# Performance work log

Hardware: AMD Instinct MI355X
Metric: run time of the kernel (lower is better)

Reference implementation:

```python
import jax, jax.numpy as jnp
import numpy as np

D = 1024
H = 16
HD = D // H
DFF = 4 * D
LN_EPS = 1e-5

def layernorm(x, gamma, beta):
    mu = jnp.mean(x, axis=-1, keepdims=True)
    var = jnp.mean(jnp.square(x - mu), axis=-1, keepdims=True)
    return (x - mu) * jax.lax.rsqrt(var + LN_EPS) * gamma + beta

def setup_inputs() -> dict:
    key = jax.random.key(0)
    ks = jax.random.split(key, 10)
    B, Nq, Nk = 2, 2048, 2048
    s = 0.02
    return {
        "q_x": jax.random.normal(ks[0], (B, Nq, D), jnp.float32),
        "kv_x": jax.random.normal(ks[1], (B, Nk, D), jnp.float32),
        "Wq": jax.random.normal(ks[2], (D, D), jnp.float32) * s,
        "Wkv": jax.random.normal(ks[3], (2 * D, D), jnp.float32) * s,
        "Wo": jax.random.normal(ks[4], (D, D), jnp.float32) * s,
        "bo": jnp.zeros((D,), jnp.float32),
        "ln_q_g": jnp.ones((D,), jnp.float32),
        "ln_q_b": jnp.zeros((D,), jnp.float32),
        "ln_kv_g": jnp.ones((D,), jnp.float32),
        "ln_kv_b": jnp.zeros((D,), jnp.float32),
        "W1": jax.random.normal(ks[5], (DFF, D), jnp.float32) * s,
        "b1": jnp.zeros((DFF,), jnp.float32),
        "W2": jax.random.normal(ks[6], (D, DFF), jnp.float32) * s,
        "b2": jnp.zeros((D,), jnp.float32),
    }

def reference(q_x, kv_x, Wq, Wkv, Wo, bo, ln_q_g, ln_q_b, ln_kv_g, ln_kv_b, W1, b1, W2, b2):
    B, Nq, _ = q_x.shape
    Nk = kv_x.shape[1]
    scale = HD ** -0.5
    # norm + projections
    q = layernorm(q_x, ln_q_g, ln_q_b) @ Wq.T                    # [B,Nq,D]
    kv = layernorm(kv_x, ln_kv_g, ln_kv_b) @ Wkv.T               # [B,Nk,2D]
    q = q.reshape(B, Nq, H, HD).transpose(0, 2, 1, 3)            # [B,H,Nq,hd]
    kv = kv.reshape(B, Nk, 2, H, HD).transpose(2, 0, 3, 1, 4)    # [2,B,H,Nk,hd]
    k, v = kv[0], kv[1]
    attn = jnp.einsum('bhqd,bhkd->bhqk', q, k) * scale           # [B,H,Nq,Nk]
    attn = jax.nn.softmax(attn, axis=-1)
    out = jnp.einsum('bhqk,bhkd->bhqd', attn, v)
    out = out.transpose(0, 2, 1, 3).reshape(B, Nq, D)
    x = q_x + out @ Wo.T + bo
    h = jax.nn.silu(x @ W1.T + b1)
    x = x + h @ W2.T + b2
    return x
```

## Files before the change

kernel.cpp:

```cpp
#include <hip/hip_runtime.h>

using u16   = unsigned short;
using f32x4 = __attribute__((ext_vector_type(4))) float;
using s16x8 = __attribute__((ext_vector_type(8))) short;
using u32x2 = __attribute__((ext_vector_type(2))) unsigned int;
using u32x4 = __attribute__((ext_vector_type(4))) unsigned int;

#define LOG2E 1.44269504088896f

static __device__ __forceinline__ u16 f2bf(float f) {
  union { float f; unsigned u; } a; a.f = f;
  unsigned r = a.u + 0x7fffu + ((a.u >> 16) & 1u);
  return (u16)(r >> 16);
}
static __device__ __forceinline__ unsigned cvtpk(float lo, float hi) {
  unsigned r;
  asm("v_cvt_pk_bf16_f32 %0, %1, %2" : "=v"(r) : "v"(lo), "v"(hi));
  return r;
}

static __device__ __forceinline__ void gload16(const void* g, void* l) {
  __builtin_amdgcn_global_load_lds(
      (__attribute__((address_space(1))) unsigned int*)g,
      (__attribute__((address_space(3))) unsigned int*)l, 16, 0, 0);
}

static __device__ __forceinline__ int xcd_swz(int b, int nb) {
  return (b & 7) * (nb >> 3) + (b >> 3);
}

__global__ __launch_bounds__(256) void prep_k(
    const float* __restrict__ Wq, const float* __restrict__ Wkv,
    const float* __restrict__ Wo, const float* __restrict__ W1,
    const float* __restrict__ W2,
    u16* __restrict__ wq_b, u16* __restrict__ wkv_b, u16* __restrict__ wo_b,
    u16* __restrict__ w1_b, u16* __restrict__ w2_b,
    const float* __restrict__ xq, const float* __restrict__ xk,
    const float* __restrict__ gq, const float* __restrict__ bq,
    const float* __restrict__ gk, const float* __restrict__ bk,
    u16* __restrict__ oq, u16* __restrict__ ok)
{
  const int blk = blockIdx.x, t = threadIdx.x;
  if (blk < 12288) {
    const int i = blk * 256 + t;
    const float* src; u16* dst; int off; float sc = 1.0f;
    if      (i <  262144) { src = Wq;  dst = wq_b;  off = i; sc = 0.125f * LOG2E; }
    else if (i <  786432) { src = Wkv; dst = wkv_b; off = i -  262144; }
    else if (i < 1048576) { src = Wo;  dst = wo_b;  off = i -  786432; }
    else if (i < 2097152) { src = W1;  dst = w1_b;  off = i - 1048576; }
    else                  { src = W2;  dst = w2_b;  off = i - 2097152; }
    const float4 v = ((const float4*)src)[off];
    ushort4 o;
    o.x = f2bf(v.x * sc); o.y = f2bf(v.y * sc); o.z = f2bf(v.z * sc); o.w = f2bf(v.w * sc);
    ((ushort4*)dst)[off] = o;
    return;
  }
  int row = blk - 12288;
  const float* x; const float* gam; const float* bet; u16* out;
  if (row < 4096) { x = xq; gam = gq; bet = bq; out = oq; }
  else { row -= 4096; x = xk; gam = gk; bet = bk; out = ok; }
  const float4 v = ((const float4*)(x + (size_t)row * 1024))[t];
  float s  = v.x + v.y + v.z + v.w;
  float ss = v.x*v.x + v.y*v.y + v.z*v.z + v.w*v.w;
  #pragma unroll
  for (int m = 1; m < 64; m <<= 1) { s += __shfl_xor(s, m); ss += __shfl_xor(ss, m); }
  __shared__ float red[8];
  const int w = t >> 6;
  if ((t & 63) == 0) { red[w] = s; red[4 + w] = ss; }
  __syncthreads();
  s  = red[0] + red[1] + red[2] + red[3];
  ss = red[4] + red[5] + red[6] + red[7];
  const float mu   = s * (1.0f / 1024.0f);
  const float rstd = rsqrtf(ss * (1.0f / 1024.0f) - mu * mu + 1e-5f);
  const float4 gv = ((const float4*)gam)[t];
  const float4 bv = ((const float4*)bet)[t];
  ushort4 o;
  o.x = f2bf((v.x - mu) * rstd * gv.x + bv.x);
  o.y = f2bf((v.y - mu) * rstd * gv.y + bv.y);
  o.z = f2bf((v.z - mu) * rstd * gv.z + bv.z);
  o.w = f2bf((v.w - mu) * rstd * gv.w + bv.w);
  ((ushort4*)(out + (size_t)row * 1024))[t] = o;
}

template<int BIAS, int RES, int SILU, int OF32, int OBF>
static __device__ __forceinline__ void gemm_body64_2buf(
    const u16* __restrict__ A, const u16* __restrict__ B,
    u16* __restrict__ Cb, float* __restrict__ Cf,
    const float* __restrict__ bias, const float* __restrict__ resid,
    int N, int K, int bid, u16* smem)
{
  const int tid = threadIdx.x;
  const int w = tid >> 6, l = tid & 63;
  const int g = l >> 4, q = l & 15;
  const int ntn = N >> 6;
  const int bm = bid / ntn, bn = bid - bm * ntn;
  const int wr = w >> 1, wc = w & 1;
  const int sw = (q & 7) << 4;
  f32x4 acc[2][2] = {};

  const size_t abase = (size_t)(bm * 128) * K;
  const size_t bbase = (size_t)(bn * 64) * K;

  auto stage = [&](int buf, int k0) {
    u16* as = smem + buf * 8192;
    u16* bs = smem + 16384 + buf * 4096;
    #pragma unroll
    for (int r = 0; r < 2; ++r) {
      const int c = (r << 9) + tid;
      const int row = c >> 3;
      const int sp = (c & 7) ^ (row & 7);
      gload16(A + abase + (size_t)row * K + k0 + sp * 8,
              as + (size_t)((r << 9) + (w << 6)) * 8);
    }
    const int row = tid >> 3;
    const int sp = (tid & 7) ^ (row & 7);
    gload16(B + bbase + (size_t)row * K + k0 + sp * 8,
            bs + (size_t)(w << 6) * 8);
  };

  const int NT = K >> 6;
  stage(0, 0);
  asm volatile("s_waitcnt vmcnt(0)" ::: "memory");
  __syncthreads();
  int cur = 0;
  for (int t = 0; t < NT; ++t) {
    if (t + 1 < NT) stage(cur ^ 1, (t + 1) << 6);
    const char* as = (const char*)(smem + cur * 8192);
    const char* bs = (const char*)(smem + 16384 + cur * 4096);
    #pragma unroll
    for (int ks = 0; ks < 2; ++ks) {
      s16x8 af[2], bfr[2];
      #pragma unroll
      for (int m = 0; m < 2; ++m)
        af[m] = *(const s16x8*)(as + (size_t)(wr * 32 + m * 16 + q) * 128 +
                                ((ks * 64 + g * 16) ^ sw));
      #pragma unroll
      for (int n = 0; n < 2; ++n)
        bfr[n] = *(const s16x8*)(bs + (size_t)(wc * 32 + n * 16 + q) * 128 +
                                 ((ks * 64 + g * 16) ^ sw));
      #pragma unroll
      for (int m = 0; m < 2; ++m)
        #pragma unroll
        for (int n = 0; n < 2; ++n)
          acc[m][n] = __builtin_amdgcn_mfma_f32_16x16x32_bf16(af[m], bfr[n], acc[m][n], 0, 0, 0);
    }
    asm volatile("s_waitcnt vmcnt(0)" ::: "memory");
    __syncthreads();
    cur ^= 1;
  }

  #pragma unroll
  for (int m = 0; m < 2; ++m) {
    const int row0 = bm * 128 + wr * 32 + m * 16 + g * 4;
    #pragma unroll
    for (int n = 0; n < 2; ++n) {
      const int col = bn * 64 + wc * 32 + n * 16 + q;
      float bv = 0.0f;
      if (BIAS) bv = bias[col];
      #pragma unroll
      for (int r = 0; r < 4; ++r) {
        const size_t idx = (size_t)(row0 + r) * N + col;
        float v = acc[m][n][r] + bv;
        if (RES)  v += resid[idx];
        if (SILU) v = v / (1.0f + __expf(-v));
        if (OF32) Cf[idx] = v;
        if (OBF)  Cb[idx] = f2bf(v);
      }
    }
  }
}

template<int BIAS, int RES, int SILU, int OF32, int OBF>
__global__ __launch_bounds__(512, 4) void gemm_k2(
    const u16* __restrict__ A, const u16* __restrict__ B,
    u16* __restrict__ Cb, float* __restrict__ Cf,
    const float* __restrict__ bias, const float* __restrict__ resid,
    int N, int K)
{
  __shared__ u16 smem[24576];
  const int bid = xcd_swz(blockIdx.x, gridDim.x);
  gemm_body64_2buf<BIAS, RES, SILU, OF32, OBF>(A, B, Cb, Cf, bias, resid, N, K, bid, smem);
}

__global__ __launch_bounds__(512, 4) void gemm_qkv_k(
    const u16* __restrict__ lnq, const u16* __restrict__ wq, u16* __restrict__ qp,
    const u16* __restrict__ lnk, const u16* __restrict__ wkv, u16* __restrict__ kvp)
{
  __shared__ u16 smem[24576];
  const int sbid = xcd_swz(blockIdx.x, 1536);
  if (sbid < 512)
    gemm_body64_2buf<0,0,0,0,1>(lnq, wq, qp, nullptr, nullptr, nullptr, 1024, 1024,
                                sbid, smem);
  else
    gemm_body64_2buf<0,0,0,0,1>(lnk, wkv, kvp, nullptr, nullptr, nullptr, 2048, 1024,
                                sbid - 512, smem);
}

template<int BIAS, int RES, int SILU, int OF32, int OBF>
__global__ __launch_bounds__(512, 4) void gemm_k3(
    const u16* __restrict__ A, const u16* __restrict__ B,
    u16* __restrict__ Cb, float* __restrict__ Cf,
    const float* __restrict__ bias, const float* __restrict__ resid,
    int N, int K)
{
  __shared__ u16 smem[36864];
  const int bid = xcd_swz(blockIdx.x, gridDim.x);
  const int tid = threadIdx.x;
  const int w = tid >> 6, l = tid & 63;
  const int g = l >> 4, q = l & 15;
  const int ntn = N >> 6;
  const int bm = bid / ntn, bn = bid - bm * ntn;
  const int wr = w >> 1, wc = w & 1;
  const int sw = (q & 7) << 4;
  f32x4 acc[2][2] = {};

  const size_t abase = (size_t)(bm * 128) * K;
  const size_t bbase = (size_t)(bn * 64) * K;

  const u16* pa0; const u16* pa1; const u16* pb;
  {
    const int r0 = tid >> 3, s0 = (tid & 7) ^ (r0 & 7);
    pa0 = A + abase + (size_t)r0 * K + s0 * 8;
    const int c1 = 512 + tid;
    const int r1 = c1 >> 3, s1 = (c1 & 7) ^ (r1 & 7);
    pa1 = A + abase + (size_t)r1 * K + s1 * 8;
    const int rb = tid >> 3, sb = (tid & 7) ^ (rb & 7);
    pb = B + bbase + (size_t)rb * K + sb * 8;
  }
  const int wdo = w * 512;

  auto stage = [&](int buf, int k0) {
    gload16(pa0 + k0, smem + buf * 8192 + wdo);
    gload16(pa1 + k0, smem + buf * 8192 + 4096 + wdo);
    gload16(pb  + k0, smem + 24576 + buf * 4096 + wdo);
  };

  const int NT = K >> 6;
  stage(0, 0);
  stage(1, 64);
  int cur = 0;
  for (int t = 0; t < NT; ++t) {
    if (t + 1 < NT) asm volatile("s_waitcnt vmcnt(3)" ::: "memory");
    else            asm volatile("s_waitcnt vmcnt(0)" ::: "memory");
    __builtin_amdgcn_s_barrier();
    asm volatile("" ::: "memory");
    if (t + 2 < NT) stage((cur == 0) ? 2 : cur - 1, (t + 2) << 6);

    const char* as = (const char*)(smem + cur * 8192);
    const char* bs = (const char*)(smem + 24576 + cur * 4096);
    #pragma unroll
    for (int ks = 0; ks < 2; ++ks) {
      s16x8 af[2], bfr[2];
      #pragma unroll
      for (int m = 0; m < 2; ++m)
        af[m] = *(const s16x8*)(as + (size_t)(wr * 32 + m * 16 + q) * 128 +
                                ((ks * 64 + g * 16) ^ sw));
      #pragma unroll
      for (int n = 0; n < 2; ++n)
        bfr[n] = *(const s16x8*)(bs + (size_t)(wc * 32 + n * 16 + q) * 128 +
                                 ((ks * 64 + g * 16) ^ sw));
      __builtin_amdgcn_s_setprio(1);
      #pragma unroll
      for (int m = 0; m < 2; ++m)
        #pragma unroll
        for (int n = 0; n < 2; ++n)
          acc[m][n] = __builtin_amdgcn_mfma_f32_16x16x32_bf16(af[m], bfr[n], acc[m][n], 0, 0, 0);
      __builtin_amdgcn_s_setprio(0);
    }
    cur = (cur == 2) ? 0 : cur + 1;
  }

  #pragma unroll
  for (int m = 0; m < 2; ++m) {
    const int row0 = bm * 128 + wr * 32 + m * 16 + g * 4;
    #pragma unroll
    for (int n = 0; n < 2; ++n) {
      const int col = bn * 64 + wc * 32 + n * 16 + q;
      float bv = 0.0f;
      if (BIAS) bv = bias[col];
      #pragma unroll
      for (int r = 0; r < 4; ++r) {
        const size_t idx = (size_t)(row0 + r) * N + col;
        float v = acc[m][n][r] + bv;
        if (RES)  v += resid[idx];
        if (SILU) v = v / (1.0f + __expf(-v));
        if (OF32) Cf[idx] = v;
        if (OBF)  Cb[idx] = f2bf(v);
      }
    }
  }
}

template<int BIAS, int RES, int SILU, int OF32, int OBF>
__global__ __launch_bounds__(512, 2) void gemm256_k(
    const u16* __restrict__ A, const u16* __restrict__ B,
    u16* __restrict__ Cb, float* __restrict__ Cf,
    const float* __restrict__ bias, const float* __restrict__ resid,
    int N, int K)
{
  __shared__ u16 smem[65536];
  char* smem_c = (char*)smem;
  const int tid = threadIdx.x;
  const int w = tid >> 6, l = tid & 63;
  const int g = l >> 4, q = l & 15;
  const int wm = w >> 2, wn = w & 3;
  const int ntn = N >> 8;
  const int bid = xcd_swz(blockIdx.x, gridDim.x);
  const int bm = bid / ntn, bn = bid - bm * ntn;

  const size_t abase = (size_t)(bm * 256) * K;
  const size_t bbase = (size_t)(bn * 256) * K;

  f32x4 acc[8][4] = {};

  auto stage2 = [&](int buf, int kt, int part) {
    const int isB = part & 1, khalf = part >> 1;
    #pragma unroll
    for (int sub = 0; sub < 2; ++sub) {
      const int row  = sub * 128 + (tid >> 2);
      const int slot = (tid & 3) ^ ((row >> 1) & 3);
      const u16* src = (isB ? B + bbase : A + abase)
                     + (size_t)row * K + kt * 64 + khalf * 32 + slot * 8;
      char* dst = smem_c + buf * 65536 + isB * 32768 + khalf * 16384
                + sub * 8192 + w * 1024;
      gload16(src, dst);
    }
  };

  const int NT = K >> 6;
  stage2(0, 0, 0); stage2(0, 0, 1); stage2(0, 0, 2); stage2(0, 0, 3);
  int cur = 0;
  const int so = (g ^ ((q >> 1) & 3)) * 16;
  for (int t = 0; t < NT; ++t) {
    const bool pre = (t + 1 < NT);
    const char* base = smem_c + cur * 65536;
    #pragma unroll
    for (int ks = 0; ks < 2; ++ks) {
      if (ks == 0 || pre) asm volatile("s_waitcnt vmcnt(4)" ::: "memory");
      else                asm volatile("s_waitcnt vmcnt(0)" ::: "memory");
      asm volatile("" ::: "memory");
      __builtin_amdgcn_s_barrier();
      asm volatile("" ::: "memory");
      const char* Ab = base + ks * 16384;
      const char* Bb = base + 32768 + ks * 16384;
      s16x8 af[8], bf0[2];
      #pragma unroll
      for (int m = 0; m < 8; ++m)
        af[m] = *(const s16x8*)(Ab + (wm * 128 + m * 16 + q) * 64 + so);
      #pragma unroll
      for (int n = 0; n < 2; ++n)
        bf0[n] = *(const s16x8*)(Bb + (wn * 64 + n * 16 + q) * 64 + so);
      if (pre) stage2(cur ^ 1, t + 1, ks * 2);
      asm volatile("s_waitcnt lgkmcnt(0)" ::: "memory");
      __builtin_amdgcn_sched_barrier(0);
      __builtin_amdgcn_s_setprio(1);
      #pragma unroll
      for (int m = 0; m < 8; ++m) {
        acc[m][0] = __builtin_amdgcn_mfma_f32_16x16x32_bf16(af[m], bf0[0], acc[m][0], 0, 0, 0);
        acc[m][1] = __builtin_amdgcn_mfma_f32_16x16x32_bf16(af[m], bf0[1], acc[m][1], 0, 0, 0);
      }
      __builtin_amdgcn_s_setprio(0);
      s16x8 bf1[2];
      #pragma unroll
      for (int n = 0; n < 2; ++n)
        bf1[n] = *(const s16x8*)(Bb + (wn * 64 + (2 + n) * 16 + q) * 64 + so);
      if (pre) stage2(cur ^ 1, t + 1, ks * 2 + 1);
      asm volatile("s_waitcnt lgkmcnt(0)" ::: "memory");
      __builtin_amdgcn_sched_barrier(0);
      __builtin_amdgcn_s_setprio(1);
      #pragma unroll
      for (int m = 0; m < 8; ++m) {
        acc[m][2] = __builtin_amdgcn_mfma_f32_16x16x32_bf16(af[m], bf1[0], acc[m][2], 0, 0, 0);
        acc[m][3] = __builtin_amdgcn_mfma_f32_16x16x32_bf16(af[m], bf1[1], acc[m][3], 0, 0, 0);
      }
      __builtin_amdgcn_s_setprio(0);
    }
    cur ^= 1;
  }

  #pragma unroll
  for (int m = 0; m < 8; ++m) {
    const int row0 = bm * 256 + wm * 128 + m * 16 + g * 4;
    #pragma unroll
    for (int n = 0; n < 4; ++n) {
      const int col = bn * 256 + wn * 64 + n * 16 + q;
      float bv = 0.0f;
      if (BIAS) bv = bias[col];
      #pragma unroll
      for (int r = 0; r < 4; ++r) {
        const size_t idx = (size_t)(row0 + r) * N + col;
        float v = acc[m][n][r] + bv;
        if (RES)  v += resid[idx];
        if (SILU) v = v / (1.0f + __expf(-v));
        if (OF32) Cf[idx] = v;
        if (OBF)  Cb[idx] = f2bf(v);
      }
    }
  }
}

__global__ __launch_bounds__(512, 4) void attn_k(
    const u16* __restrict__ Q, const u16* __restrict__ KV, u16* __restrict__ O)
{
  __shared__ u16 Ks[3][64 * 64];
  __shared__ u16 Vs[3][64 * 64];
  const int tid = threadIdx.x;
  const int w = tid >> 6, l = tid & 63;
  const int g = l >> 4, q = l & 15;
  const int idx = blockIdx.x >> 3;
  const int bh = (blockIdx.x & 7) * 4 + (idx >> 4);
  const int qt = idx & 15;
  const int b = bh >> 4, h = bh & 15;

  const size_t qrow = (size_t)(b * 2048 + qt * 128 + w * 16 + q);
  s16x8 qf[2];
  qf[0] = *(const s16x8*)&Q[qrow * 1024 + h * 64 + g * 8];
  qf[1] = *(const s16x8*)&Q[qrow * 1024 + h * 64 + 32 + g * 8];

  f32x4 oacc[4] = {};
  f32x4 ls = {0.0f, 0.0f, 0.0f, 0.0f};

  const u16* kvb = KV + (size_t)b * 2048 * 2048;
  const unsigned vs_base =
      (unsigned)(unsigned long long)(__attribute__((address_space(3))) u16*)Vs;

  const u16* pk; const u16* pv;
  {
    const int krow = tid >> 3, slot = tid & 7;
    pk = kvb + (size_t)krow * 2048 + h * 64 + ((slot ^ (krow & 7)) << 3);
    const int vkv = ((tid >> 3) & 15) * 4 + ((tid >> 1) & 3);
    const int vd0 = ((tid >> 7) & 3) * 16 + (tid & 1) * 8;
    pv = kvb + (size_t)vkv * 2048 + 1024 + h * 64 + vd0;
  }
  const int wdo = w * 512;

  auto stage = [&](int buf, int kv0) {
    const size_t off = (size_t)kv0 << 11;
    gload16(pk + off, &Ks[buf][0] + wdo);
    gload16(pv + off, &Vs[buf][0] + wdo);
  };

  stage(0, 0);
  stage(1, 64);
  int cur = 0;

  for (int kt = 0; kt < 32; ++kt) {
    if (kt < 31) asm volatile("s_waitcnt vmcnt(2)" ::: "memory");
    else         asm volatile("s_waitcnt vmcnt(0)" ::: "memory");
    __builtin_amdgcn_s_barrier();
    asm volatile("" ::: "memory");
    if (kt + 2 < 32) stage((cur == 0) ? 2 : cur - 1, (kt + 2) * 64);

    const char* ksb = (const char*)Ks[cur];
    f32x4 sacc[4] = {};
    __builtin_amdgcn_s_setprio(1);
    #pragma unroll
    for (int s = 0; s < 2; ++s)
      #pragma unroll
      for (int nf = 0; nf < 4; ++nf) {
        const int krw = nf * 16 + q;
        const s16x8 kf = *(const s16x8*)(ksb + krw * 128 +
                              ((s * 64 + g * 16) ^ ((krw & 7) << 4)));
        sacc[nf] = __builtin_amdgcn_mfma_f32_16x16x32_bf16(kf, qf[s], sacc[nf], 0, 0, 0);
      }
    __builtin_amdgcn_s_setprio(0);

    #pragma unroll
    for (int nf = 0; nf < 4; ++nf)
      #pragma unroll
      for (int r = 0; r < 4; ++r)
        sacc[nf][r] = __builtin_amdgcn_exp2f(sacc[nf][r]);
    ls += sacc[0]; ls += sacc[1]; ls += sacc[2]; ls += sacc[3];

    union { u32x4 u; s16x8 s8; } au[2];
    #pragma unroll
    for (int s = 0; s < 2; ++s) {
      au[s].u[0] = cvtpk(sacc[2*s  ][0], sacc[2*s  ][1]);
      au[s].u[1] = cvtpk(sacc[2*s  ][2], sacc[2*s  ][3]);
      au[s].u[2] = cvtpk(sacc[2*s+1][0], sacc[2*s+1][1]);
      au[s].u[3] = cvtpk(sacc[2*s+1][2], sacc[2*s+1][3]);
    }

    const unsigned a0 = vs_base + (unsigned)(cur * 8192) + (unsigned)(g * 128 + 2 * q);
    u32x2 v0,v1,v2,v3,v4,v5,v6,v7,v8,v9,v10,v11,v12,v13,v14,v15;
    asm volatile(
        "ds_read_b64_tr_b16 %0,  %16\n\t"
        "ds_read_b64_tr_b16 %1,  %16 offset:512\n\t"
        "ds_read_b64_tr_b16 %2,  %16 offset:2048\n\t"
        "ds_read_b64_tr_b16 %3,  %16 offset:2560\n\t"
        "ds_read_b64_tr_b16 %4,  %16 offset:4096\n\t"
        "ds_read_b64_tr_b16 %5,  %16 offset:4608\n\t"
        "ds_read_b64_tr_b16 %6,  %16 offset:6144\n\t"
        "ds_read_b64_tr_b16 %7,  %16 offset:6656\n\t"
        "ds_read_b64_tr_b16 %8,  %16 offset:1024\n\t"
        "ds_read_b64_tr_b16 %9,  %16 offset:1536\n\t"
        "ds_read_b64_tr_b16 %10, %16 offset:3072\n\t"
        "ds_read_b64_tr_b16 %11, %16 offset:3584\n\t"
        "ds_read_b64_tr_b16 %12, %16 offset:5120\n\t"
        "ds_read_b64_tr_b16 %13, %16 offset:5632\n\t"
        "ds_read_b64_tr_b16 %14, %16 offset:7168\n\t"
        "ds_read_b64_tr_b16 %15, %16 offset:7680\n\t"
        "s_waitcnt lgkmcnt(0)"
        : "=&v"(v0), "=&v"(v1), "=&v"(v2),  "=&v"(v3),
          "=&v"(v4), "=&v"(v5), "=&v"(v6),  "=&v"(v7),
          "=&v"(v8), "=&v"(v9), "=&v"(v10), "=&v"(v11),
          "=&v"(v12),"=&v"(v13),"=&v"(v14), "=&v"(v15)
        : "v"(a0) : "memory");
    __builtin_amdgcn_sched_barrier(0);

    __builtin_amdgcn_s_setprio(1);
    {
      union { u32x4 u; s16x8 s8; } bu;
      bu.u[0]=v0[0];  bu.u[1]=v0[1];  bu.u[2]=v1[0];  bu.u[3]=v1[1];
      oacc[0] = __builtin_amdgcn_mfma_f32_16x16x32_bf16(au[0].s8, bu.s8, oacc[0], 0, 0, 0);
      bu.u[0]=v2[0];  bu.u[1]=v2[1];  bu.u[2]=v3[0];  bu.u[3]=v3[1];
      oacc[1] = __builtin_amdgcn_mfma_f32_16x16x32_bf16(au[0].s8, bu.s8, oacc[1], 0, 0, 0);
      bu.u[0]=v4[0];  bu.u[1]=v4[1];  bu.u[2]=v5[0];  bu.u[3]=v5[1];
      oacc[2] = __builtin_amdgcn_mfma_f32_16x16x32_bf16(au[0].s8, bu.s8, oacc[2], 0, 0, 0);
      bu.u[0]=v6[0];  bu.u[1]=v6[1];  bu.u[2]=v7[0];  bu.u[3]=v7[1];
      oacc[3] = __builtin_amdgcn_mfma_f32_16x16x32_bf16(au[0].s8, bu.s8, oacc[3], 0, 0, 0);
      bu.u[0]=v8[0];  bu.u[1]=v8[1];  bu.u[2]=v9[0];  bu.u[3]=v9[1];
      oacc[0] = __builtin_amdgcn_mfma_f32_16x16x32_bf16(au[1].s8, bu.s8, oacc[0], 0, 0, 0);
      bu.u[0]=v10[0]; bu.u[1]=v10[1]; bu.u[2]=v11[0]; bu.u[3]=v11[1];
      oacc[1] = __builtin_amdgcn_mfma_f32_16x16x32_bf16(au[1].s8, bu.s8, oacc[1], 0, 0, 0);
      bu.u[0]=v12[0]; bu.u[1]=v12[1]; bu.u[2]=v13[0]; bu.u[3]=v13[1];
      oacc[2] = __builtin_amdgcn_mfma_f32_16x16x32_bf16(au[1].s8, bu.s8, oacc[2], 0, 0, 0);
      bu.u[0]=v14[0]; bu.u[1]=v14[1]; bu.u[2]=v15[0]; bu.u[3]=v15[1];
      oacc[3] = __builtin_amdgcn_mfma_f32_16x16x32_bf16(au[1].s8, bu.s8, oacc[3], 0, 0, 0);
    }
    __builtin_amdgcn_s_setprio(0);

    cur = (cur == 2) ? 0 : cur + 1;
  }

  float lsum = (ls[0] + ls[1]) + (ls[2] + ls[3]);
  lsum += __shfl_xor(lsum, 16);
  lsum += __shfl_xor(lsum, 32);
  float lr[4];
  #pragma unroll
  for (int r = 0; r < 4; ++r) lr[r] = __shfl(lsum, g * 4 + r);
  const size_t ob = (size_t)(b * 2048 + qt * 128 + w * 16) * 1024 + h * 64;
  #pragma unroll
  for (int r = 0; r < 4; ++r) {
    const float inv = 1.0f / lr[r];
    #pragma unroll
    for (int nf = 0; nf < 4; ++nf)
      O[ob + (size_t)(g * 4 + r) * 1024 + nf * 16 + q] = f2bf(oacc[nf][r] * inv);
  }
}

extern "C" void kernel_launch(void* const* d_in, const int* in_sizes, int n_in,
                              void* d_out, int out_size, void* d_ws, size_t ws_size,
                              hipStream_t stream)
{
  const float* q_x  = (const float*)d_in[0];
  const float* kv_x = (const float*)d_in[1];
  const float* Wq   = (const float*)d_in[2];
  const float* Wkv  = (const float*)d_in[3];
  const float* Wo   = (const float*)d_in[4];
  const float* bo   = (const float*)d_in[5];
  const float* lnqg = (const float*)d_in[6];
  const float* lnqb = (const float*)d_in[7];
  const float* lnkg = (const float*)d_in[8];
  const float* lnkb = (const float*)d_in[9];
  const float* W1   = (const float*)d_in[10];
  const float* b1   = (const float*)d_in[11];
  const float* W2   = (const float*)d_in[12];
  const float* b2   = (const float*)d_in[13];
  float* out = (float*)d_out;

  char* ws = (char*)d_ws;
  const size_t MB = 1024 * 1024;
  u16*   wq_b  = (u16*)  (ws +  0 * MB);
  u16*   wkv_b = (u16*)  (ws +  2 * MB);
  u16*   wo_b  = (u16*)  (ws +  6 * MB);
  u16*   w1_b  = (u16*)  (ws +  8 * MB);
  u16*   w2_b  = (u16*)  (ws + 16 * MB);
  u16*   lnq   = (u16*)  (ws + 24 * MB);
  u16*   lnk   = (u16*)  (ws + 32 * MB);
  u16*   qp    = (u16*)  (ws + 40 * MB);
  u16*   kvp   = (u16*)  (ws + 48 * MB);
  u16*   ao    = (u16*)  (ws + 64 * MB);
  float* xf    = (float*)(ws + 72 * MB);
  u16*   xb    = (u16*)  (ws + 88 * MB);
  u16*   hb    = (u16*)  (ws + 96 * MB);

  prep_k<<<dim3(20480), dim3(256), 0, stream>>>(
      Wq, Wkv, Wo, W1, W2, wq_b, wkv_b, wo_b, w1_b, w2_b,
      q_x, kv_x, lnqg, lnqb, lnkg, lnkb, lnq, lnk);

  gemm_qkv_k<<<dim3(1536), dim3(512), 0, stream>>>(lnq, wq_b, qp, lnk, wkv_b, kvp);
  attn_k<<<dim3(512), dim3(512), 0, stream>>>(qp, kvp, ao);
  gemm_k2<1,1,0,1,1><<<dim3(512),  dim3(512), 0, stream>>>(
      ao, wo_b, xb, xf, bo, q_x, 1024, 1024);
  gemm256_k<1,0,1,0,1><<<dim3(256), dim3(512), 0, stream>>>(
      xb, w1_b, hb, nullptr, b1, nullptr, 4096, 1024);
  gemm_k3<1,1,0,1,0><<<dim3(512),  dim3(512), 0, stream>>>(
      hb, w2_b, nullptr, out, b2, xf, 1024, 4096);
}
```

Baseline: 193.6 us.

## Stage 128-row KV tiles with double buffering instead of 64-row triple buffering

The attention kernel now loads 128 keys and values per pipeline stage into two LDS buffers, instead of 64 keys into three buffers. Each stage is processed as two 64-row halves. This halves the number of barriers and waitcnt synchronisation points per KV sweep. The cost is a shallower prefetch: each iteration now waits on vmcnt(0), so all loads must complete before compute starts, which can expose global-load latency. LDS use rises from 48KB to 64KB per block, which may limit occupancy at 4 blocks per CU.

```diff
diff --git a/kernel.cpp b/kernel.cpp
--- a/kernel.cpp
+++ b/kernel.cpp
@@ -402,8 +402,8 @@
 __global__ __launch_bounds__(512, 4) void attn_k(
     const u16* __restrict__ Q, const u16* __restrict__ KV, u16* __restrict__ O)
 {
-  __shared__ u16 Ks[3][64 * 64];
-  __shared__ u16 Vs[3][64 * 64];
+  __shared__ u16 Ks[2][128 * 64];
+  __shared__ u16 Vs[2][128 * 64];
   const int tid = threadIdx.x;
   const int w = tid >> 6, l = tid & 63;
   const int g = l >> 4, q = l & 15;
@@ -424,113 +424,120 @@
   const unsigned vs_base =
       (unsigned)(unsigned long long)(__attribute__((address_space(3))) u16*)Vs;
 
-  const u16* pk; const u16* pv;
+  const u16 *pk0, *pk1, *pv0, *pv1;
   {
-    const int krow = tid >> 3, slot = tid & 7;
-    pk = kvb + (size_t)krow * 2048 + h * 64 + ((slot ^ (krow & 7)) << 3);
+    int c = tid, krow = c >> 3, slot = c & 7;
+    pk0 = kvb + (size_t)krow * 2048 + h * 64 + ((slot ^ (krow & 7)) << 3);
+    c = 512 + tid; krow = c >> 3; slot = c & 7;
+    pk1 = kvb + (size_t)krow * 2048 + h * 64 + ((slot ^ (krow & 7)) << 3);
     const int vkv = ((tid >> 3) & 15) * 4 + ((tid >> 1) & 3);
     const int vd0 = ((tid >> 7) & 3) * 16 + (tid & 1) * 8;
-    pv = kvb + (size_t)vkv * 2048 + 1024 + h * 64 + vd0;
+    pv0 = kvb + (size_t)vkv * 2048 + 1024 + h * 64 + vd0;
+    pv1 = pv0 + (size_t)64 * 2048;
   }
   const int wdo = w * 512;
 
   auto stage = [&](int buf, int kv0) {
     const size_t off = (size_t)kv0 << 11;
-    gload16(pk + off, &Ks[buf][0] + wdo);
-    gload16(pv + off, &Vs[buf][0] + wdo);
+    gload16(pk0 + off, &Ks[buf][0]    + wdo);
+    gload16(pk1 + off, &Ks[buf][4096] + wdo);
+    gload16(pv0 + off, &Vs[buf][0]    + wdo);
+    gload16(pv1 + off, &Vs[buf][4096] + wdo);
   };
 
   stage(0, 0);
-  stage(1, 64);
   int cur = 0;
 
-  for (int kt = 0; kt < 32; ++kt) {
-    if (kt < 31) asm volatile("s_waitcnt vmcnt(2)" ::: "memory");
-    else         asm volatile("s_waitcnt vmcnt(0)" ::: "memory");
+  for (int kt = 0; kt < 16; ++kt) {
+    asm volatile("s_waitcnt vmcnt(0)" ::: "memory");
     __builtin_amdgcn_s_barrier();
     asm volatile("" ::: "memory");
-    if (kt + 2 < 32) stage((cur == 0) ? 2 : cur - 1, (kt + 2) * 64);
-
-    const char* ksb = (const char*)Ks[cur];
-    f32x4 sacc[4] = {};
-    __builtin_amdgcn_s_setprio(1);
-    #pragma unroll
-    for (int s = 0; s < 2; ++s)
-      #pragma unroll
-      for (int nf = 0; nf < 4; ++nf) {
-        const int krw = nf * 16 + q;
-        const s16x8 kf = *(const s16x8*)(ksb + krw * 128 +
-                              ((s * 64 + g * 16) ^ ((krw & 7) << 4)));
-        sacc[nf] = __builtin_amdgcn_mfma_f32_16x16x32_bf16(kf, qf[s], sacc[nf], 0, 0, 0);
+    if (kt + 1 < 16) stage(cur ^ 1, (kt + 1) * 128);
+
+    #pragma unroll
+    for (int hh = 0; hh < 2; ++hh) {
+      const char* ksb = (const char*)Ks[cur] + hh * 8192;
+      f32x4 sacc[4] = {};
+      __builtin_amdgcn_s_setprio(1);
+      #pragma unroll
+      for (int s = 0; s < 2; ++s)
+        #pragma unroll
+        for (int nf = 0; nf < 4; ++nf) {
+          const int krw = nf * 16 + q;
+          const s16x8 kf = *(const s16x8*)(ksb + krw * 128 +
+                                ((s * 64 + g * 16) ^ ((krw & 7) << 4)));
+          sacc[nf] = __builtin_amdgcn_mfma_f32_16x16x32_bf16(kf, qf[s], sacc[nf], 0, 0, 0);
+        }
+      __builtin_amdgcn_s_setprio(0);
+
+      #pragma unroll
+      for (int nf = 0; nf < 4; ++nf)
+        #pragma unroll
+        for (int r = 0; r < 4; ++r)
+          sacc[nf][r] = __builtin_amdgcn_exp2f(sacc[nf][r]);
+      ls += sacc[0]; ls += sacc[1]; ls += sacc[2]; ls += sacc[3];
+
+      union { u32x4 u; s16x8 s8; } au[2];
+      #pragma unroll
+      for (int s = 0; s < 2; ++s) {
+        au[s].u[0] = cvtpk(sacc[2*s  ][0], sacc[2*s  ][1]);
+        au[s].u[1] = cvtpk(sacc[2*s  ][2], sacc[2*s  ][3]);
+        au[s].u[2] = cvtpk(sacc[2*s+1][0], sacc[2*s+1][1]);
+        au[s].u[3] = cvtpk(sacc[2*s+1][2], sacc[2*s+1][3]);
       }
-    __builtin_amdgcn_s_setprio(0);
-
-    #pragma unroll
-    for (int nf = 0; nf < 4; ++nf)
-      #pragma unroll
-      for (int r = 0; r < 4; ++r)
-        sacc[nf][r] = __builtin_amdgcn_exp2f(sacc[nf][r]);
-    ls += sacc[0]; ls += sacc[1]; ls += sacc[2]; ls += sacc[3];
-
-    union { u32x4 u; s16x8 s8; } au[2];
-    #pragma unroll
-    for (int s = 0; s < 2; ++s) {
-      au[s].u[0] = cvtpk(sacc[2*s  ][0], sacc[2*s  ][1]);
-      au[s].u[1] = cvtpk(sacc[2*s  ][2], sacc[2*s  ][3]);
-      au[s].u[2] = cvtpk(sacc[2*s+1][0], sacc[2*s+1][1]);
-      au[s].u[3] = cvtpk(sacc[2*s+1][2], sacc[2*s+1][3]);
-    }
-
-    const unsigned a0 = vs_base + (unsigned)(cur * 8192) + (unsigned)(g * 128 + 2 * q);
-    u32x2 v0,v1,v2,v3,v4,v5,v6,v7,v8,v9,v10,v11,v12,v13,v14,v15;
-    asm volatile(
-        "ds_read_b64_tr_b16 %0,  %16\n\t"
-        "ds_read_b64_tr_b16 %1,  %16 offset:512\n\t"
-        "ds_read_b64_tr_b16 %2,  %16 offset:2048\n\t"
-        "ds_read_b64_tr_b16 %3,  %16 offset:2560\n\t"
-        "ds_read_b64_tr_b16 %4,  %16 offset:4096\n\t"
-        "ds_read_b64_tr_b16 %5,  %16 offset:4608\n\t"
-        "ds_read_b64_tr_b16 %6,  %16 offset:6144\n\t"
-        "ds_read_b64_tr_b16 %7,  %16 offset:6656\n\t"
-        "ds_read_b64_tr_b16 %8,  %16 offset:1024\n\t"
-        "ds_read_b64_tr_b16 %9,  %16 offset:1536\n\t"
-        "ds_read_b64_tr_b16 %10, %16 offset:3072\n\t"
-        "ds_read_b64_tr_b16 %11, %16 offset:3584\n\t"
-        "ds_read_b64_tr_b16 %12, %16 offset:5120\n\t"
-        "ds_read_b64_tr_b16 %13, %16 offset:5632\n\t"
-        "ds_read_b64_tr_b16 %14, %16 offset:7168\n\t"
-        "ds_read_b64_tr_b16 %15, %16 offset:7680\n\t"
-        "s_waitcnt lgkmcnt(0)"
-        : "=&v"(v0), "=&v"(v1), "=&v"(v2),  "=&v"(v3),
-          "=&v"(v4), "=&v"(v5), "=&v"(v6),  "=&v"(v7),
-          "=&v"(v8), "=&v"(v9), "=&v"(v10), "=&v"(v11),
-          "=&v"(v12),"=&v"(v13),"=&v"(v14), "=&v"(v15)
-        : "v"(a0) : "memory");
-    __builtin_amdgcn_sched_barrier(0);
-
-    __builtin_amdgcn_s_setprio(1);
-    {
-      union { u32x4 u; s16x8 s8; } bu;
-      bu.u[0]=v0[0];  bu.u[1]=v0[1];  bu.u[2]=v1[0];  bu.u[3]=v1[1];
-      oacc[0] = __builtin_amdgcn_mfma_f32_16x16x32_bf16(au[0].s8, bu.s8, oacc[0], 0, 0, 0);
-      bu.u[0]=v2[0];  bu.u[1]=v2[1];  bu.u[2]=v3[0];  bu.u[3]=v3[1];
-      oacc[1] = __builtin_amdgcn_mfma_f32_16x16x32_bf16(au[0].s8, bu.s8, oacc[1], 0, 0, 0);
-      bu.u[0]=v4[0];  bu.u[1]=v4[1];  bu.u[2]=v5[0];  bu.u[3]=v5[1];
-      oacc[2] = __builtin_amdgcn_mfma_f32_16x16x32_bf16(au[0].s8, bu.s8, oacc[2], 0, 0, 0);
-      bu.u[0]=v6[0];  bu.u[1]=v6[1];  bu.u[2]=v7[0];  bu.u[3]=v7[1];
-      oacc[3] = __builtin_amdgcn_mfma_f32_16x16x32_bf16(au[0].s8, bu.s8, oacc[3], 0, 0, 0);
-      bu.u[0]=v8[0];  bu.u[1]=v8[1];  bu.u[2]=v9[0];  bu.u[3]=v9[1];
-      oacc[0] = __builtin_amdgcn_mfma_f32_16x16x32_bf16(au[1].s8, bu.s8, oacc[0], 0, 0, 0);
-      bu.u[0]=v10[0]; bu.u[1]=v10[1]; bu.u[2]=v11[0]; bu.u[3]=v11[1];
-      oacc[1] = __builtin_amdgcn_mfma_f32_16x16x32_bf16(au[1].s8, bu.s8, oacc[1], 0, 0, 0);
-      bu.u[0]=v12[0]; bu.u[1]=v12[1]; bu.u[2]=v13[0]; bu.u[3]=v13[1];
-      oacc[2] = __builtin_amdgcn_mfma_f32_16x16x32_bf16(au[1].s8, bu.s8, oacc[2], 0, 0, 0);
-      bu.u[0]=v14[0]; bu.u[1]=v14[1]; bu.u[2]=v15[0]; bu.u[3]=v15[1];
-      oacc[3] = __builtin_amdgcn_mfma_f32_16x16x32_bf16(au[1].s8, bu.s8, oacc[3], 0, 0, 0);
-    }
-    __builtin_amdgcn_s_setprio(0);
-
-    cur = (cur == 2) ? 0 : cur + 1;
+
+      const unsigned a0 = vs_base + (unsigned)(cur * 16384 + hh * 8192)
+                        + (unsigned)(g * 128 + 2 * q);
+      u32x2 v0,v1,v2,v3,v4,v5,v6,v7,v8,v9,v10,v11,v12,v13,v14,v15;
+      asm volatile(
+          "ds_read_b64_tr_b16 %0,  %16\n\t"
+          "ds_read_b64_tr_b16 %1,  %16 offset:512\n\t"
+          "ds_read_b64_tr_b16 %2,  %16 offset:2048\n\t"
+          "ds_read_b64_tr_b16 %3,  %16 offset:2560\n\t"
+          "ds_read_b64_tr_b16 %4,  %16 offset:4096\n\t"
+          "ds_read_b64_tr_b16 %5,  %16 offset:4608\n\t"
+          "ds_read_b64_tr_b16 %6,  %16 offset:6144\n\t"
+          "ds_read_b64_tr_b16 %7,  %16 offset:6656\n\t"
+          "ds_read_b64_tr_b16 %8,  %16 offset:1024\n\t"
+          "ds_read_b64_tr_b16 %9,  %16 offset:1536\n\t"
+          "ds_read_b64_tr_b16 %10, %16 offset:3072\n\t"
+          "ds_read_b64_tr_b16 %11, %16 offset:3584\n\t"
+          "ds_read_b64_tr_b16 %12, %16 offset:5120\n\t"
+          "ds_read_b64_tr_b16 %13, %16 offset:5632\n\t"
+          "ds_read_b64_tr_b16 %14, %16 offset:7168\n\t"
+          "ds_read_b64_tr_b16 %15, %16 offset:7680\n\t"
+          "s_waitcnt lgkmcnt(0)"
+          : "=&v"(v0), "=&v"(v1), "=&v"(v2),  "=&v"(v3),
+            "=&v"(v4), "=&v"(v5), "=&v"(v6),  "=&v"(v7),
+            "=&v"(v8), "=&v"(v9), "=&v"(v10), "=&v"(v11),
+            "=&v"(v12),"=&v"(v13),"=&v"(v14), "=&v"(v15)
+          : "v"(a0) : "memory");
+      __builtin_amdgcn_sched_barrier(0);
+
+      __builtin_amdgcn_s_setprio(1);
+      {
+        union { u32x4 u; s16x8 s8; } bu;
+        bu.u[0]=v0[0];  bu.u[1]=v0[1];  bu.u[2]=v1[0];  bu.u[3]=v1[1];
+        oacc[0] = __builtin_amdgcn_mfma_f32_16x16x32_bf16(au[0].s8, bu.s8, oacc[0], 0, 0, 0);
+        bu.u[0]=v2[0];  bu.u[1]=v2[1];  bu.u[2]=v3[0];  bu.u[3]=v3[1];
+        oacc[1] = __builtin_amdgcn_mfma_f32_16x16x32_bf16(au[0].s8, bu.s8, oacc[1], 0, 0, 0);
+        bu.u[0]=v4[0];  bu.u[1]=v4[1];  bu.u[2]=v5[0];  bu.u[3]=v5[1];
+        oacc[2] = __builtin_amdgcn_mfma_f32_16x16x32_bf16(au[0].s8, bu.s8, oacc[2], 0, 0, 0);
+        bu.u[0]=v6[0];  bu.u[1]=v6[1];  bu.u[2]=v7[0];  bu.u[3]=v7[1];
+        oacc[3] = __builtin_amdgcn_mfma_f32_16x16x32_bf16(au[0].s8, bu.s8, oacc[3], 0, 0, 0);
+        bu.u[0]=v8[0];  bu.u[1]=v8[1];  bu.u[2]=v9[0];  bu.u[3]=v9[1];
+        oacc[0] = __builtin_amdgcn_mfma_f32_16x16x32_bf16(au[1].s8, bu.s8, oacc[0], 0, 0, 0);
+        bu.u[0]=v10[0]; bu.u[1]=v10[1]; bu.u[2]=v11[0]; bu.u[3]=v11[1];
+        oacc[1] = __builtin_amdgcn_mfma_f32_16x16x32_bf16(au[1].s8, bu.s8, oacc[1], 0, 0, 0);
+        bu.u[0]=v12[0]; bu.u[1]=v12[1]; bu.u[2]=v13[0]; bu.u[3]=v13[1];
+        oacc[2] = __builtin_amdgcn_mfma_f32_16x16x32_bf16(au[1].s8, bu.s8, oacc[2], 0, 0, 0);
+        bu.u[0]=v14[0]; bu.u[1]=v14[1]; bu.u[2]=v15[0]; bu.u[3]=v15[1];
+        oacc[3] = __builtin_amdgcn_mfma_f32_16x16x32_bf16(au[1].s8, bu.s8, oacc[3], 0, 0, 0);
+      }
+      __builtin_amdgcn_s_setprio(0);
+    }
+
+    cur ^= 1;
   }
 
   float lsum = (ls[0] + ls[1]) + (ls[2] + ls[3]);
```

Result: no change. 194.1 us (+0.3%).
